# Performance work log

Measured on AMD Instinct MI355X. Metric: run time of the kernel, lower is better.

## Reference

```python
import jax, jax.numpy as jnp
import numpy as np

B, N, C, D, T = 16, 1024, 16, 64, 32  # batch, max_size, max_n_colors, inner_dim, timesteps


def setup_inputs() -> dict:
    key = jax.random.key(0)
    ks = jax.random.split(key, 16)
    s = 1.0 / np.sqrt(D)
    inp = {
        "Mvv": jax.random.randint(ks[0], (B, N, N), 0, 2).astype(jnp.float32),
        "n_colors": jax.random.randint(ks[1], (B,), 2, C + 1),
        # learned / initial states
        "v_init": jax.random.normal(ks[2], (D,)) * s,            # Normal(0,1)/sqrt(D)
        "ch0": jax.random.uniform(ks[3], (B, C, D)),             # Uniform(0,1) color init
        # recurrent GNN weights (simple tanh message-passing RNN)
        "W_v": jax.random.normal(ks[4], (D, D)) * s,
        "W_vv": jax.random.normal(ks[5], (D, D)) * s,
        "W_vc": jax.random.normal(ks[6], (D, D)) * s,
        "b_v": jnp.zeros((D,)),
        "W_c": jax.random.normal(ks[7], (D, D)) * s,
        "W_cv": jax.random.normal(ks[8], (D, D)) * s,
        "b_c": jnp.zeros((D,)),
        # vote MLP: Linear(D, D//4) -> Sigmoid -> Linear(D//4, 1)
        "W1": jax.random.normal(ks[9], (D, D // 4)) * s,
        "b1": jnp.zeros((D // 4,)),
        "W2": jax.random.normal(ks[10], (D // 4, 1)) * (1.0 / np.sqrt(D // 4)),
        "b2": jnp.zeros((1,)),
    }
    return inp


def reference(Mvv, n_colors, v_init, ch0, W_v, W_vv, W_vc, b_v, W_c, W_cv, b_c, W1, b1, W2, b2):
    # add self loops (Mvv += eye)
    A = Mvv + jnp.eye(N, dtype=Mvv.dtype)[None]
    # vectorized Mvc: Mvc[b, i, j] = 1 if j < n_colors[b]
    Mvc = jnp.broadcast_to(
        (jnp.arange(C)[None, None, :] < n_colors[:, None, None]).astype(Mvv.dtype),
        (B, N, C),
    )
    # hidden state init: v_init repeated over batch/nodes
    vh0 = jnp.broadcast_to(v_init, (B, N, D))

    def step(carry, _):
        vh, ch = carry
        v_agg = jnp.einsum("bnm,bmd->bnd", A, vh)      # neighbor aggregation
        c_agg = jnp.einsum("bnc,bcd->bnd", Mvc, ch)    # color -> vertex messages
        vh_new = jnp.tanh(vh @ W_v + v_agg @ W_vv + c_agg @ W_vc + b_v)
        cv_agg = jnp.einsum("bnc,bnd->bcd", Mvc, vh_new)  # vertex -> color messages
        ch_new = jnp.tanh(ch @ W_c + cv_agg @ W_cv + b_c)
        return (vh_new, ch_new), None

    (vh, _), _ = jax.lax.scan(step, (vh0, ch0), None, length=T)

    # vote MLP + mean over nodes + sigmoid
    vote = jax.nn.sigmoid(vh @ W1 + b1) @ W2 + b2      # [B, N, 1]
    pred = jax.nn.sigmoid(jnp.mean(vote, axis=1)).squeeze()  # [B]
    return pred
```

## Files before the change

### kernel.cpp

```cpp
#include <hip/hip_runtime.h>
#include <hip/hip_bf16.h>
#include <math.h>

#define BB 16
#define NN 1024
#define CC 16
#define DD 64
#define TT 32

typedef __bf16 bf16;
typedef __bf16 bf16x8 __attribute__((ext_vector_type(8)));
typedef __bf16 bf16x4 __attribute__((ext_vector_type(4)));
typedef float f32x4 __attribute__((ext_vector_type(4)));
typedef unsigned int u32;
typedef unsigned long long u64;
typedef u32 u32v4 __attribute__((ext_vector_type(4)));

__device__ __forceinline__ void split2(float x, bf16& h, bf16& l) {
    h = (bf16)x;
    l = (bf16)(x - (float)h);
}

__device__ __forceinline__ float fast_tanh(float x) {
    float ax = fabsf(x);
    float e = __expf(-2.f * ax);
    float t = 1.f - 2.f * e / (1.f + e);
    return copysignf(t, x);
}

__device__ __forceinline__ bf16x8 expand_bits(u32 b8) {
    u32 w[4];
    #pragma unroll
    for (int p = 0; p < 4; ++p) {
        u32 tt = b8 >> (2 * p);
        w[p] = ((tt & 1u) | ((tt & 2u) << 15)) * 0x3F80u;
    }
    u32v4 u = { w[0], w[1], w[2], w[3] };
    return __builtin_bit_cast(bf16x8, u);
}


__global__ __launch_bounds__(256) void prep_kernel(
    const float* __restrict__ Mvv, const float* __restrict__ v_init,
    const float* __restrict__ W_v, const float* __restrict__ W_vv,
    u64* __restrict__ Abits,
    bf16* __restrict__ vhHi, bf16* __restrict__ vhLo,
    bf16* __restrict__ VfHi, bf16* __restrict__ VfLo,
    bf16* __restrict__ WvTh, bf16* __restrict__ WvTl,
    bf16* __restrict__ WvvTh, bf16* __restrict__ WvvTl)
{
    int gid = blockIdx.x, tid = threadIdx.x;
    if (gid < 4096) {
        int w = tid >> 6, lane = tid & 63;
        for (int it = 0; it < 16; ++it) {
            int W = gid * 64 + w * 16 + it;
            int bb  = W >> 14;
            int row = (W >> 4) & 1023;
            int wq  = W & 15;
            float x = Mvv[(((size_t)bb << 10) + row) * 1024 + wq * 64 + lane];
            u64 m = __ballot(x != 0.0f);
            if (lane == 0) Abits[W] = m;
        }
    } else if (gid < 4608) {
        size_t idx = ((size_t)(gid - 4096) * 256 + tid) * 8;
        int d0 = (int)(idx & (DD - 1));
        bf16x8 oh, ol;
        #pragma unroll
        for (int e = 0; e < 8; ++e) { bf16 h, l; split2(v_init[d0 + e], h, l); oh[e] = h; ol[e] = l; }
        *(bf16x8*)(vhHi + idx) = oh;
        *(bf16x8*)(vhLo + idx) = ol;
    } else if (gid < 5120) {
        size_t idx = ((size_t)(gid - 4608) * 256 + tid) * 8;
        int j = (int)((idx >> 5) & 63);
        bf16 h, l; split2(v_init[j], h, l);
        bf16x8 oh, ol;
        #pragma unroll
        for (int e = 0; e < 8; ++e) { oh[e] = h; ol[e] = l; }
        *(bf16x8*)(VfHi + idx) = oh;
        *(bf16x8*)(VfLo + idx) = ol;
    } else {
        for (int e = tid; e < DD * DD; e += 256) {
            int n = e >> 6, k = e & 63;
            bf16 h, l;
            split2(W_v[k * DD + n], h, l);
            WvTh[e] = h; WvTl[e] = l;
            split2(W_vv[k * DD + n], h, l);
            WvvTh[e] = h; WvvTl[e] = l;
        }
    }
}

__global__ __launch_bounds__(512, 2) void step_kernel(
    const u64* __restrict__ Abits,
    const bf16* __restrict__ vhHi_in, const bf16* __restrict__ vhLo_in,
    const bf16* __restrict__ VfHi_in, const bf16* __restrict__ VfLo_in,
    bf16* __restrict__ vhHi_out, bf16* __restrict__ vhLo_out,
    bf16* __restrict__ VfHi_out, bf16* __restrict__ VfLo_out,
    const float* __restrict__ ch_in, float* __restrict__ ch_out,
    const float* __restrict__ part_prev, float* __restrict__ part_out,
    const int* __restrict__ n_colors,
    const float* __restrict__ Wc, const float* __restrict__ Wcv, const float* __restrict__ bc,
    const float* __restrict__ Wvc, const float* __restrict__ bv,
    const bf16* __restrict__ WvTh, const bf16* __restrict__ WvTl,
    const bf16* __restrict__ WvvTh, const bf16* __restrict__ WvvTl,
    const float* __restrict__ W1, const float* __restrict__ b1, const float* __restrict__ W2,
    float* __restrict__ partial,
    int t)
{
    __shared__ float sWc[4096];
    __shared__ float sChI[1024];
    __shared__ float sRed[512];
    __shared__ float sBc[64], sBv[64], sVs[64], sMv[64], sCs[64], sCv[64];
    __shared__ float vagg[2][64 * 65];

    int tid  = threadIdx.x;
    int b    = blockIdx.x & 15;
    int blkr = blockIdx.x >> 4;
    int m0   = blkr * 64;
    int ncol = n_colors[b];
    int d = tid & 63, q = tid >> 6;

    for (int e = tid; e < 4096; e += 512) sWc[e] = Wc[e];
    for (int e = tid; e < 1024; e += 512) sChI[e] = ch_in[(size_t)b * 1024 + e];
    if (tid < 64) { sBc[tid] = bc[tid]; sBv[tid] = bv[tid]; }

    float pr[8];
    if (t > 0) {
        #pragma unroll
        for (int j = 0; j < 8; ++j)
            pr[j] = part_prev[(size_t)b * 4096 + (q * 8 + j) * 64 + d];
    }

    int lane = tid & 63, w = tid >> 6;
    int l16 = lane & 15, lhi = lane >> 4;
    int wm = w & 1, wn = (w >> 1) & 1, wk = w >> 2;

    f32x4 acc[2][2];
    #pragma unroll
    for (int mi = 0; mi < 2; ++mi)
        #pragma unroll
        for (int nt = 0; nt < 2; ++nt) acc[mi][nt] = (f32x4){0.f, 0.f, 0.f, 0.f};

    const u64* Ab = Abits + ((size_t)b * NN + m0 + wm * 32 + l16) * 16 + wk * 8;
    const bf16* VfH = VfHi_in + (size_t)b * 65536;
    const bf16* VfL = VfLo_in + (size_t)b * 65536;

    #pragma unroll
    for (int kt = 0; kt < 4; ++kt) {
        u32v4 aw0 = *(const u32v4*)(Ab + kt * 2);
        u32v4 aw1 = *(const u32v4*)(Ab + 256 + kt * 2);
        #pragma unroll
        for (int kk = 0; kk < 4; ++kk) {
            int ks = wk * 16 + kt * 4 + kk;
            bf16x8 a0 = expand_bits((aw0[kk] >> (lhi * 8)) & 0xFFu);
            bf16x8 a1 = expand_bits((aw1[kk] >> (lhi * 8)) & 0xFFu);
            size_t fo = (size_t)ks * 2048 + (wn * 32 + l16) * 32 + lhi * 8;
            bf16x8 bh0 = *(const bf16x8*)(VfH + fo);
            bf16x8 bl0 = *(const bf16x8*)(VfL + fo);
            bf16x8 bh1 = *(const bf16x8*)(VfH + fo + 512);
            bf16x8 bl1 = *(const bf16x8*)(VfL + fo + 512);
            acc[0][0] = __builtin_amdgcn_mfma_f32_16x16x32_bf16(a0, bh0, acc[0][0], 0, 0, 0);
            acc[0][1] = __builtin_amdgcn_mfma_f32_16x16x32_bf16(a0, bh1, acc[0][1], 0, 0, 0);
            acc[1][0] = __builtin_amdgcn_mfma_f32_16x16x32_bf16(a1, bh0, acc[1][0], 0, 0, 0);
            acc[1][1] = __builtin_amdgcn_mfma_f32_16x16x32_bf16(a1, bh1, acc[1][1], 0, 0, 0);
            acc[0][0] = __builtin_amdgcn_mfma_f32_16x16x32_bf16(a0, bl0, acc[0][0], 0, 0, 0);
            acc[0][1] = __builtin_amdgcn_mfma_f32_16x16x32_bf16(a0, bl1, acc[0][1], 0, 0, 0);
            acc[1][0] = __builtin_amdgcn_mfma_f32_16x16x32_bf16(a1, bl0, acc[1][0], 0, 0, 0);
            acc[1][1] = __builtin_amdgcn_mfma_f32_16x16x32_bf16(a1, bl1, acc[1][1], 0, 0, 0);
        }
    }

    #pragma unroll
    for (int mi = 0; mi < 2; ++mi)
        #pragma unroll
        for (int nt = 0; nt < 2; ++nt)
            #pragma unroll
            for (int r = 0; r < 4; ++r)
                vagg[wk][(wm * 32 + mi * 16 + lhi * 4 + r) * 65 + wn * 32 + nt * 16 + l16] = acc[mi][nt][r];
    __syncthreads();

    if (t > 0) {
        {
            float s = 0.f;
            #pragma unroll
            for (int j = 0; j < 8; ++j) s += pr[j];
            sRed[tid] = s;
        }
        __syncthreads();
        if (tid < 64) {
            float v = 0.f;
            #pragma unroll
            for (int i = 0; i < 8; ++i) v += sRed[tid + 64 * i];
            sVs[tid] = v;
        }
        __syncthreads();
        {
            float pm = 0.f;
            #pragma unroll
            for (int j = 0; j < 8; ++j) { int k = q * 8 + j; pm += sVs[k] * Wcv[k * 64 + d]; }
            sRed[tid] = pm;
        }
        __syncthreads();
        if (tid < 64) {
            float v = 0.f;
            #pragma unroll
            for (int i = 0; i < 8; ++i) v += sRed[tid + 64 * i];
            sMv[tid] = v;
        }
        __syncthreads();
        float cn[2];
        #pragma unroll
        for (int ci = 0; ci < 2; ++ci) {
            int c = q * 2 + ci;
            float s = sBc[d] + ((c < ncol) ? sMv[d] : 0.f);
            for (int k = 0; k < 64; ++k) s += sChI[c * 64 + k] * sWc[k * 64 + d];
            cn[ci] = fast_tanh(s);
        }
        __syncthreads();
        #pragma unroll
        for (int ci = 0; ci < 2; ++ci) {
            int c = q * 2 + ci;
            sChI[c * 64 + d] = cn[ci];
            ch_out[(size_t)b * 1024 + c * 64 + d] = cn[ci];
        }
        __syncthreads();
    }
    {
        float pcs = 0.f;
        #pragma unroll
        for (int ci = 0; ci < 2; ++ci) { int c = q * 2 + ci; if (c < ncol) pcs += sChI[c * 64 + d]; }
        sRed[tid] = pcs;
    }
    __syncthreads();
    if (tid < 64) {
        float v = 0.f;
        #pragma unroll
        for (int i = 0; i < 8; ++i) v += sRed[tid + 64 * i];
        sCs[tid] = v;
    }
    __syncthreads();
    {
        float pv = 0.f;
        #pragma unroll
        for (int j = 0; j < 8; ++j) { int k = q * 8 + j; pv += sCs[k] * Wvc[k * 64 + d]; }
        sRed[tid] = pv;
    }
    __syncthreads();
    if (tid < 64) {
        float v = sBv[tid];
        #pragma unroll
        for (int i = 0; i < 8; ++i) v += sRed[tid + 64 * i];
        sCv[tid] = v;
    }
    __syncthreads();

    int rt = (w & 3) * 16, ct = (w >> 2) * 32;

    f32x4 p2[2][2];
    #pragma unroll
    for (int nt = 0; nt < 2; ++nt)
        #pragma unroll
        for (int kk = 0; kk < 2; ++kk) p2[nt][kk] = (f32x4){0.f, 0.f, 0.f, 0.f};

    #pragma unroll
    for (int kk = 0; kk < 2; ++kk) {
        int d0 = kk * 32 + lhi * 8;
        size_t vo = ((size_t)b * NN + m0 + rt + l16) * 64 + d0;
        bf16x8 a1h = *(const bf16x8*)(vhHi_in + vo);
        bf16x8 a1l = *(const bf16x8*)(vhLo_in + vo);
        int vb = (rt + l16) * 65 + d0;
        bf16x8 a2h, a2l;
        #pragma unroll
        for (int e = 0; e < 8; ++e) {
            float v = vagg[0][vb + e] + vagg[1][vb + e] + (float)a1h[e] + (float)a1l[e];
            bf16 h, l; split2(v, h, l);
            a2h[e] = h; a2l[e] = l;
        }
        #pragma unroll
        for (int nt = 0; nt < 2; ++nt) {
            int woff = (ct + nt * 16 + l16) * 64 + d0;
            bf16x8 b1h = *(const bf16x8*)(WvTh + woff);
            bf16x8 b1l = *(const bf16x8*)(WvTl + woff);
            bf16x8 b2h = *(const bf16x8*)(WvvTh + woff);
            bf16x8 b2l = *(const bf16x8*)(WvvTl + woff);
            p2[nt][kk] = __builtin_amdgcn_mfma_f32_16x16x32_bf16(a1h, b1h, p2[nt][kk], 0, 0, 0);
            p2[nt][kk] = __builtin_amdgcn_mfma_f32_16x16x32_bf16(a1l, b1h, p2[nt][kk], 0, 0, 0);
            p2[nt][kk] = __builtin_amdgcn_mfma_f32_16x16x32_bf16(a1h, b1l, p2[nt][kk], 0, 0, 0);
            p2[nt][kk] = __builtin_amdgcn_mfma_f32_16x16x32_bf16(a2h, b2h, p2[nt][kk], 0, 0, 0);
            p2[nt][kk] = __builtin_amdgcn_mfma_f32_16x16x32_bf16(a2l, b2h, p2[nt][kk], 0, 0, 0);
            p2[nt][kk] = __builtin_amdgcn_mfma_f32_16x16x32_bf16(a2h, b2l, p2[nt][kk], 0, 0, 0);
        }
    }

    float tvv[2][4];
    #pragma unroll
    for (int nt = 0; nt < 2; ++nt) {
        float cv = sCv[ct + nt * 16 + l16];
        #pragma unroll
        for (int r = 0; r < 4; ++r) tvv[nt][r] = fast_tanh(p2[nt][0][r] + p2[nt][1][r] + cv);
    }

    if (t < TT - 1) {
        int ksW = (m0 + rt) >> 5;
        int khi = 2 * ((rt >> 4) & 1) + (lhi >> 1);
        size_t vout_base = (size_t)b * NN * DD;
        #pragma unroll
        for (int nt = 0; nt < 2; ++nt) {
            int col = ct + nt * 16 + l16;
            float cs = tvv[nt][0] + tvv[nt][1] + tvv[nt][2] + tvv[nt][3];
            cs += __shfl_xor(cs, 16);
            cs += __shfl_xor(cs, 32);
            if (lhi == 0)
                part_out[(((size_t)b * 16 + blkr) * 4 + (w & 3)) * 64 + col] = cs;

            bf16x4 pkh, pkl;
            #pragma unroll
            for (int r = 0; r < 4; ++r) {
                bf16 h, l; split2(tvv[nt][r], h, l);
                pkh[r] = h; pkl[r] = l;
                size_t ro = vout_base + (size_t)(m0 + rt + lhi * 4 + r) * 64 + col;
                vhHi_out[ro] = h;
                vhLo_out[ro] = l;
            }
            size_t fo = (size_t)b * 65536 + (size_t)ksW * 2048 + col * 32 + khi * 8 + (lhi & 1) * 4;
            *(bf16x4*)(VfHi_out + fo) = pkh;
            *(bf16x4*)(VfLo_out + fo) = pkl;
        }
    } else {
        __syncthreads();
        float* sX  = &vagg[0][0];
        float* sW1 = &vagg[1][0];
        #pragma unroll
        for (int nt = 0; nt < 2; ++nt) {
            int col = ct + nt * 16 + l16;
            #pragma unroll
            for (int r = 0; r < 4; ++r)
                sX[(rt + lhi * 4 + r) * 65 + col] = tvv[nt][r];
        }
        for (int e = tid; e < 1024; e += 512) sW1[e] = W1[e];
        if (tid < 16) { sVs[tid] = W2[tid]; sMv[tid] = b1[tid]; }
        __syncthreads();

        int nl = tid & 63;
        int jq = tid >> 6;
        float h0 = sMv[jq * 2], h1 = sMv[jq * 2 + 1];
        for (int dd = 0; dd < 64; ++dd) {
            float x = sX[nl * 65 + dd];
            h0 += x * sW1[dd * 16 + jq * 2];
            h1 += x * sW1[dd * 16 + jq * 2 + 1];
        }
        float pv = sVs[jq * 2] / (1.f + __expf(-h0)) + sVs[jq * 2 + 1] / (1.f + __expf(-h1));
        sRed[tid] = pv;
        __syncthreads();
        if (tid < 64) {
            float v = 0.f;
            #pragma unroll
            for (int i = 0; i < 8; ++i) v += sRed[tid + 64 * i];
            #pragma unroll
            for (int off = 1; off < 64; off <<= 1) v += __shfl_xor(v, off);
            if (tid == 0) partial[blockIdx.x] = v;
        }
    }
}

__global__ __launch_bounds__(256) void final_reduce_kernel(
    const float* __restrict__ partial, const float* __restrict__ b2, float* __restrict__ out)
{
    int tid = threadIdx.x;
    int b = tid >> 4, p = tid & 15;
    float v = partial[p * 16 + b];
    #pragma unroll
    for (int off = 1; off < 16; off <<= 1) v += __shfl_xor(v, off);
    if (p == 0) out[b] = 1.f / (1.f + expf(-(v / 1024.f + b2[0])));
}

extern "C" void kernel_launch(void* const* d_in, const int* in_sizes, int n_in,
                              void* d_out, int out_size, void* d_ws, size_t ws_size,
                              hipStream_t stream) {
    const float* Mvv  = (const float*)d_in[0];
    const int*   ncol = (const int*)d_in[1];
    const float* vini = (const float*)d_in[2];
    const float* ch0  = (const float*)d_in[3];
    const float* W_v  = (const float*)d_in[4];
    const float* W_vv = (const float*)d_in[5];
    const float* W_vc = (const float*)d_in[6];
    const float* b_v  = (const float*)d_in[7];
    const float* W_c  = (const float*)d_in[8];
    const float* W_cv = (const float*)d_in[9];
    const float* b_c  = (const float*)d_in[10];
    const float* W1   = (const float*)d_in[11];
    const float* b1   = (const float*)d_in[12];
    const float* W2   = (const float*)d_in[13];
    const float* b2   = (const float*)d_in[14];

    char* base = (char*)d_ws;
    size_t off = 0;
    u64* Abits = (u64*)(base + off); off += (size_t)BB * NN * 16 * 8;
    const size_t SVH = (size_t)BB * NN * DD * 2;
    bf16* vhHi[2] = {(bf16*)(base + off), (bf16*)(base + off + SVH)}; off += 2 * SVH;
    bf16* vhLo[2] = {(bf16*)(base + off), (bf16*)(base + off + SVH)}; off += 2 * SVH;
    bf16* VfHi[2] = {(bf16*)(base + off), (bf16*)(base + off + SVH)}; off += 2 * SVH;
    bf16* VfLo[2] = {(bf16*)(base + off), (bf16*)(base + off + SVH)}; off += 2 * SVH;
    const size_t SCH = (size_t)BB * CC * DD * 4;
    float* chb[2] = {(float*)(base + off), (float*)(base + off + SCH)}; off += 2 * SCH;
    const size_t SPB = (size_t)BB * 64 * DD * 4;
    float* pb[2] = {(float*)(base + off), (float*)(base + off + SPB)}; off += 2 * SPB;
    bf16* WvTh  = (bf16*)(base + off); off += DD * DD * 2;
    bf16* WvTl  = (bf16*)(base + off); off += DD * DD * 2;
    bf16* WvvTh = (bf16*)(base + off); off += DD * DD * 2;
    bf16* WvvTl = (bf16*)(base + off); off += DD * DD * 2;
    float* partial = (float*)(base + off); off += 256 * 4;

    prep_kernel<<<5121, 256, 0, stream>>>(Mvv, vini, W_v, W_vv, Abits,
        vhHi[0], vhLo[0], VfHi[0], VfLo[0], WvTh, WvTl, WvvTh, WvvTl);

    for (int t = 0; t < TT; ++t) {
        const float* ch_in = (t <= 1) ? ch0 : chb[(t - 1) & 1];
        int i = t & 1, o = (t + 1) & 1;
        step_kernel<<<256, 512, 0, stream>>>(Abits,
            vhHi[i], vhLo[i], VfHi[i], VfLo[i],
            vhHi[o], vhLo[o], VfHi[o], VfLo[o],
            ch_in, chb[t & 1],
            pb[(t + 1) & 1], pb[t & 1],
            ncol, W_c, W_cv, b_c, W_vc, b_v,
            WvTh, WvTl, WvvTh, WvvTl,
            W1, b1, W2, partial, t);
    }

    final_reduce_kernel<<<1, 256, 0, stream>>>(partial, b2, (float*)d_out);
}
```

Measured before the change: 703.0 us.

## Halve rows per block and double the step kernel grid

The step kernel now handles 32 vertex rows per block instead of 64, so it launches 512 blocks instead of 256 and asks for higher occupancy in its launch bounds. The warp-to-tile mapping for the aggregation matmul and the dense-update matmul is reworked so each wave owns a single 16-column tile. The partial-sum layout and the vote reduction, including the final reduce kernel, are adjusted to match. The aim is to spread each latency-bound timestep over more waves and CUs, at the cost of repeating the per-batch colour and weight setup (Wc load, colour reductions) in twice as many blocks.

```diff
diff --git a/kernel.cpp b/kernel.cpp
--- a/kernel.cpp
+++ b/kernel.cpp
@@ -90,7 +90,7 @@
     }
 }
 
-__global__ __launch_bounds__(512, 2) void step_kernel(
+__global__ __launch_bounds__(512, 4) void step_kernel(
     const u64* __restrict__ Abits,
     const bf16* __restrict__ vhHi_in, const bf16* __restrict__ vhLo_in,
     const bf16* __restrict__ VfHi_in, const bf16* __restrict__ VfLo_in,
@@ -111,12 +111,12 @@
     __shared__ float sChI[1024];
     __shared__ float sRed[512];
     __shared__ float sBc[64], sBv[64], sVs[64], sMv[64], sCs[64], sCv[64];
-    __shared__ float vagg[2][64 * 65];
+    __shared__ float vagg[2][32 * 65];
 
     int tid  = threadIdx.x;
     int b    = blockIdx.x & 15;
     int blkr = blockIdx.x >> 4;
-    int m0   = blkr * 64;
+    int m0   = blkr * 32;
     int ncol = n_colors[b];
     int d = tid & 63, q = tid >> 6;
 
@@ -133,15 +133,13 @@
 
     int lane = tid & 63, w = tid >> 6;
     int l16 = lane & 15, lhi = lane >> 4;
-    int wm = w & 1, wn = (w >> 1) & 1, wk = w >> 2;
-
-    f32x4 acc[2][2];
-    #pragma unroll
-    for (int mi = 0; mi < 2; ++mi)
-        #pragma unroll
-        for (int nt = 0; nt < 2; ++nt) acc[mi][nt] = (f32x4){0.f, 0.f, 0.f, 0.f};
-
-    const u64* Ab = Abits + ((size_t)b * NN + m0 + wm * 32 + l16) * 16 + wk * 8;
+    int wn = w & 3, wk = w >> 2;
+
+    f32x4 acc[2];
+    acc[0] = (f32x4){0.f, 0.f, 0.f, 0.f};
+    acc[1] = (f32x4){0.f, 0.f, 0.f, 0.f};
+
+    const u64* Ab = Abits + ((size_t)b * NN + m0 + l16) * 16 + wk * 8;
     const bf16* VfH = VfHi_in + (size_t)b * 65536;
     const bf16* VfL = VfLo_in + (size_t)b * 65536;
 
@@ -154,29 +152,21 @@
             int ks = wk * 16 + kt * 4 + kk;
             bf16x8 a0 = expand_bits((aw0[kk] >> (lhi * 8)) & 0xFFu);
             bf16x8 a1 = expand_bits((aw1[kk] >> (lhi * 8)) & 0xFFu);
-            size_t fo = (size_t)ks * 2048 + (wn * 32 + l16) * 32 + lhi * 8;
-            bf16x8 bh0 = *(const bf16x8*)(VfH + fo);
-            bf16x8 bl0 = *(const bf16x8*)(VfL + fo);
-            bf16x8 bh1 = *(const bf16x8*)(VfH + fo + 512);
-            bf16x8 bl1 = *(const bf16x8*)(VfL + fo + 512);
-            acc[0][0] = __builtin_amdgcn_mfma_f32_16x16x32_bf16(a0, bh0, acc[0][0], 0, 0, 0);
-            acc[0][1] = __builtin_amdgcn_mfma_f32_16x16x32_bf16(a0, bh1, acc[0][1], 0, 0, 0);
-            acc[1][0] = __builtin_amdgcn_mfma_f32_16x16x32_bf16(a1, bh0, acc[1][0], 0, 0, 0);
-            acc[1][1] = __builtin_amdgcn_mfma_f32_16x16x32_bf16(a1, bh1, acc[1][1], 0, 0, 0);
-            acc[0][0] = __builtin_amdgcn_mfma_f32_16x16x32_bf16(a0, bl0, acc[0][0], 0, 0, 0);
-            acc[0][1] = __builtin_amdgcn_mfma_f32_16x16x32_bf16(a0, bl1, acc[0][1], 0, 0, 0);
-            acc[1][0] = __builtin_amdgcn_mfma_f32_16x16x32_bf16(a1, bl0, acc[1][0], 0, 0, 0);
-            acc[1][1] = __builtin_amdgcn_mfma_f32_16x16x32_bf16(a1, bl1, acc[1][1], 0, 0, 0);
+            size_t fo = (size_t)ks * 2048 + (wn * 16 + l16) * 32 + lhi * 8;
+            bf16x8 bh = *(const bf16x8*)(VfH + fo);
+            bf16x8 bl = *(const bf16x8*)(VfL + fo);
+            acc[0] = __builtin_amdgcn_mfma_f32_16x16x32_bf16(a0, bh, acc[0], 0, 0, 0);
+            acc[1] = __builtin_amdgcn_mfma_f32_16x16x32_bf16(a1, bh, acc[1], 0, 0, 0);
+            acc[0] = __builtin_amdgcn_mfma_f32_16x16x32_bf16(a0, bl, acc[0], 0, 0, 0);
+            acc[1] = __builtin_amdgcn_mfma_f32_16x16x32_bf16(a1, bl, acc[1], 0, 0, 0);
         }
     }
 
     #pragma unroll
     for (int mi = 0; mi < 2; ++mi)
         #pragma unroll
-        for (int nt = 0; nt < 2; ++nt)
-            #pragma unroll
-            for (int r = 0; r < 4; ++r)
-                vagg[wk][(wm * 32 + mi * 16 + lhi * 4 + r) * 65 + wn * 32 + nt * 16 + l16] = acc[mi][nt][r];
+        for (int r = 0; r < 4; ++r)
+            vagg[wk][(mi * 16 + lhi * 4 + r) * 65 + wn * 16 + l16] = acc[mi][r];
     __syncthreads();
 
     if (t > 0) {
@@ -254,13 +244,9 @@
     }
     __syncthreads();
 
-    int rt = (w & 3) * 16, ct = (w >> 2) * 32;
-
-    f32x4 p2[2][2];
-    #pragma unroll
-    for (int nt = 0; nt < 2; ++nt)
-        #pragma unroll
-        for (int kk = 0; kk < 2; ++kk) p2[nt][kk] = (f32x4){0.f, 0.f, 0.f, 0.f};
+    int rt = (w & 1) * 16, ct = (w >> 1) * 16;
+
+    f32x4 p2 = (f32x4){0.f, 0.f, 0.f, 0.f};
 
     #pragma unroll
     for (int kk = 0; kk < 2; ++kk) {
@@ -276,101 +262,84 @@
             bf16 h, l; split2(v, h, l);
             a2h[e] = h; a2l[e] = l;
         }
-        #pragma unroll
-        for (int nt = 0; nt < 2; ++nt) {
-            int woff = (ct + nt * 16 + l16) * 64 + d0;
-            bf16x8 b1h = *(const bf16x8*)(WvTh + woff);
-            bf16x8 b1l = *(const bf16x8*)(WvTl + woff);
-            bf16x8 b2h = *(const bf16x8*)(WvvTh + woff);
-            bf16x8 b2l = *(const bf16x8*)(WvvTl + woff);
-            p2[nt][kk] = __builtin_amdgcn_mfma_f32_16x16x32_bf16(a1h, b1h, p2[nt][kk], 0, 0, 0);
-            p2[nt][kk] = __builtin_amdgcn_mfma_f32_16x16x32_bf16(a1l, b1h, p2[nt][kk], 0, 0, 0);
-            p2[nt][kk] = __builtin_amdgcn_mfma_f32_16x16x32_bf16(a1h, b1l, p2[nt][kk], 0, 0, 0);
-            p2[nt][kk] = __builtin_amdgcn_mfma_f32_16x16x32_bf16(a2h, b2h, p2[nt][kk], 0, 0, 0);
-            p2[nt][kk] = __builtin_amdgcn_mfma_f32_16x16x32_bf16(a2l, b2h, p2[nt][kk], 0, 0, 0);
-            p2[nt][kk] = __builtin_amdgcn_mfma_f32_16x16x32_bf16(a2h, b2l, p2[nt][kk], 0, 0, 0);
-        }
-    }
-
-    float tvv[2][4];
-    #pragma unroll
-    for (int nt = 0; nt < 2; ++nt) {
-        float cv = sCv[ct + nt * 16 + l16];
-        #pragma unroll
-        for (int r = 0; r < 4; ++r) tvv[nt][r] = fast_tanh(p2[nt][0][r] + p2[nt][1][r] + cv);
-    }
+        int woff = (ct + l16) * 64 + d0;
+        bf16x8 b1h = *(const bf16x8*)(WvTh + woff);
+        bf16x8 b1l = *(const bf16x8*)(WvTl + woff);
+        bf16x8 b2h = *(const bf16x8*)(WvvTh + woff);
+        bf16x8 b2l = *(const bf16x8*)(WvvTl + woff);
+        p2 = __builtin_amdgcn_mfma_f32_16x16x32_bf16(a1h, b1h, p2, 0, 0, 0);
+        p2 = __builtin_amdgcn_mfma_f32_16x16x32_bf16(a1l, b1h, p2, 0, 0, 0);
+        p2 = __builtin_amdgcn_mfma_f32_16x16x32_bf16(a1h, b1l, p2, 0, 0, 0);
+        p2 = __builtin_amdgcn_mfma_f32_16x16x32_bf16(a2h, b2h, p2, 0, 0, 0);
+        p2 = __builtin_amdgcn_mfma_f32_16x16x32_bf16(a2l, b2h, p2, 0, 0, 0);
+        p2 = __builtin_amdgcn_mfma_f32_16x16x32_bf16(a2h, b2l, p2, 0, 0, 0);
+    }
+
+    int col = ct + l16;
+    float cv = sCv[col];
+    float tv[4];
+    #pragma unroll
+    for (int r = 0; r < 4; ++r) tv[r] = fast_tanh(p2[r] + cv);
 
     if (t < TT - 1) {
+        float cs = tv[0] + tv[1] + tv[2] + tv[3];
+        cs += __shfl_xor(cs, 16);
+        cs += __shfl_xor(cs, 32);
+        if (lhi == 0)
+            part_out[(size_t)b * 4096 + (blkr * 2 + (w & 1)) * 64 + col] = cs;
+
+        size_t vout_base = (size_t)b * NN * DD;
+        bf16x4 pkh, pkl;
+        #pragma unroll
+        for (int r = 0; r < 4; ++r) {
+            bf16 h, l; split2(tv[r], h, l);
+            pkh[r] = h; pkl[r] = l;
+            size_t ro = vout_base + (size_t)(m0 + rt + lhi * 4 + r) * 64 + col;
+            vhHi_out[ro] = h;
+            vhLo_out[ro] = l;
+        }
         int ksW = (m0 + rt) >> 5;
         int khi = 2 * ((rt >> 4) & 1) + (lhi >> 1);
-        size_t vout_base = (size_t)b * NN * DD;
-        #pragma unroll
-        for (int nt = 0; nt < 2; ++nt) {
-            int col = ct + nt * 16 + l16;
-            float cs = tvv[nt][0] + tvv[nt][1] + tvv[nt][2] + tvv[nt][3];
-            cs += __shfl_xor(cs, 16);
-            cs += __shfl_xor(cs, 32);
-            if (lhi == 0)
-                part_out[(((size_t)b * 16 + blkr) * 4 + (w & 3)) * 64 + col] = cs;
-
-            bf16x4 pkh, pkl;
-            #pragma unroll
-            for (int r = 0; r < 4; ++r) {
-                bf16 h, l; split2(tvv[nt][r], h, l);
-                pkh[r] = h; pkl[r] = l;
-                size_t ro = vout_base + (size_t)(m0 + rt + lhi * 4 + r) * 64 + col;
-                vhHi_out[ro] = h;
-                vhLo_out[ro] = l;
-            }
-            size_t fo = (size_t)b * 65536 + (size_t)ksW * 2048 + col * 32 + khi * 8 + (lhi & 1) * 4;
-            *(bf16x4*)(VfHi_out + fo) = pkh;
-            *(bf16x4*)(VfLo_out + fo) = pkl;
-        }
+        size_t fo = (size_t)b * 65536 + (size_t)ksW * 2048 + col * 32 + khi * 8 + (lhi & 1) * 4;
+        *(bf16x4*)(VfHi_out + fo) = pkh;
+        *(bf16x4*)(VfLo_out + fo) = pkl;
     } else {
         __syncthreads();
         float* sX  = &vagg[0][0];
         float* sW1 = &vagg[1][0];
         #pragma unroll
-        for (int nt = 0; nt < 2; ++nt) {
-            int col = ct + nt * 16 + l16;
-            #pragma unroll
-            for (int r = 0; r < 4; ++r)
-                sX[(rt + lhi * 4 + r) * 65 + col] = tvv[nt][r];
-        }
+        for (int r = 0; r < 4; ++r)
+            sX[(rt + lhi * 4 + r) * 65 + col] = tv[r];
         for (int e = tid; e < 1024; e += 512) sW1[e] = W1[e];
         if (tid < 16) { sVs[tid] = W2[tid]; sMv[tid] = b1[tid]; }
         __syncthreads();
 
-        int nl = tid & 63;
-        int jq = tid >> 6;
-        float h0 = sMv[jq * 2], h1 = sMv[jq * 2 + 1];
-        for (int dd = 0; dd < 64; ++dd) {
-            float x = sX[nl * 65 + dd];
-            h0 += x * sW1[dd * 16 + jq * 2];
-            h1 += x * sW1[dd * 16 + jq * 2 + 1];
-        }
-        float pv = sVs[jq * 2] / (1.f + __expf(-h0)) + sVs[jq * 2 + 1] / (1.f + __expf(-h1));
-        sRed[tid] = pv;
-        __syncthreads();
-        if (tid < 64) {
-            float v = 0.f;
-            #pragma unroll
-            for (int i = 0; i < 8; ++i) v += sRed[tid + 64 * i];
-            #pragma unroll
-            for (int off = 1; off < 64; off <<= 1) v += __shfl_xor(v, off);
-            if (tid == 0) partial[blockIdx.x] = v;
-        }
-    }
-}
-
-__global__ __launch_bounds__(256) void final_reduce_kernel(
+        int nl = tid & 31;
+        int jq = tid >> 5;
+        float h = sMv[jq];
+        for (int dd = 0; dd < 64; ++dd)
+            h += sX[nl * 65 + dd] * sW1[dd * 16 + jq];
+        sRed[jq * 32 + nl] = sVs[jq] / (1.f + __expf(-h));
+        __syncthreads();
+        if (tid < 32) {
+            float vote = 0.f;
+            #pragma unroll
+            for (int j = 0; j < 16; ++j) vote += sRed[j * 32 + tid];
+            #pragma unroll
+            for (int off = 1; off < 32; off <<= 1) vote += __shfl_xor(vote, off);
+            if (tid == 0) partial[blockIdx.x] = vote;
+        }
+    }
+}
+
+__global__ __launch_bounds__(512) void final_reduce_kernel(
     const float* __restrict__ partial, const float* __restrict__ b2, float* __restrict__ out)
 {
     int tid = threadIdx.x;
-    int b = tid >> 4, p = tid & 15;
+    int b = tid >> 5, p = tid & 31;
     float v = partial[p * 16 + b];
     #pragma unroll
-    for (int off = 1; off < 16; off <<= 1) v += __shfl_xor(v, off);
+    for (int off = 1; off < 32; off <<= 1) v += __shfl_xor(v, off);
     if (p == 0) out[b] = 1.f / (1.f + expf(-(v / 1024.f + b2[0])));
 }
 
@@ -409,7 +378,7 @@
     bf16* WvTl  = (bf16*)(base + off); off += DD * DD * 2;
     bf16* WvvTh = (bf16*)(base + off); off += DD * DD * 2;
     bf16* WvvTl = (bf16*)(base + off); off += DD * DD * 2;
-    float* partial = (float*)(base + off); off += 256 * 4;
+    float* partial = (float*)(base + off); off += 512 * 4;
 
     prep_kernel<<<5121, 256, 0, stream>>>(Mvv, vini, W_v, W_vv, Abits,
         vhHi[0], vhLo[0], VfHi[0], VfLo[0], WvTh, WvTl, WvvTh, WvvTl);
@@ -417,7 +386,7 @@
     for (int t = 0; t < TT; ++t) {
         const float* ch_in = (t <= 1) ? ch0 : chb[(t - 1) & 1];
         int i = t & 1, o = (t + 1) & 1;
-        step_kernel<<<256, 512, 0, stream>>>(Abits,
+        step_kernel<<<512, 512, 0, stream>>>(Abits,
             vhHi[i], vhLo[i], VfHi[i], VfLo[i],
             vhHi[o], vhLo[o], VfHi[o], VfLo[o],
             ch_in, chb[t & 1],
@@ -427,5 +396,5 @@
             W1, b1, W2, partial, t);
     }
 
-    final_reduce_kernel<<<1, 256, 0, stream>>>(partial, b2, (float*)d_out);
-}
+    final_reduce_kernel<<<1, 512, 0, stream>>>(partial, b2, (float*)d_out);
+}
```

Measured after the change: 941.6 us. +33.9%, slower.

## Compute color-state update in a single wave with shuffles instead of block-wide reductions

Applied to the files above, without the earlier changes.

Moves the per-step color hidden-state update and color-to-vertex message computation into wave 0, using register arrays and lane shuffles. This replaces the shared-memory staging of Wc, the 8-way block reductions and about ten __syncthreads barriers. It also makes only block row 0 write ch_out rather than every block. The trade-off is that one wave does all this serial work while the other waves wait at the barrier, and shared memory use drops, which may allow more blocks per CU.

```diff
diff --git a/kernel.cpp b/kernel.cpp
--- a/kernel.cpp
+++ b/kernel.cpp
@@ -107,29 +107,15 @@
     float* __restrict__ partial,
     int t)
 {
-    __shared__ float sWc[4096];
-    __shared__ float sChI[1024];
+    __shared__ float vagg[2][64 * 65];
     __shared__ float sRed[512];
-    __shared__ float sBc[64], sBv[64], sVs[64], sMv[64], sCs[64], sCv[64];
-    __shared__ float vagg[2][64 * 65];
+    __shared__ float sCv[64], sVs[64], sMv[64];
 
     int tid  = threadIdx.x;
     int b    = blockIdx.x & 15;
     int blkr = blockIdx.x >> 4;
     int m0   = blkr * 64;
     int ncol = n_colors[b];
-    int d = tid & 63, q = tid >> 6;
-
-    for (int e = tid; e < 4096; e += 512) sWc[e] = Wc[e];
-    for (int e = tid; e < 1024; e += 512) sChI[e] = ch_in[(size_t)b * 1024 + e];
-    if (tid < 64) { sBc[tid] = bc[tid]; sBv[tid] = bv[tid]; }
-
-    float pr[8];
-    if (t > 0) {
-        #pragma unroll
-        for (int j = 0; j < 8; ++j)
-            pr[j] = part_prev[(size_t)b * 4096 + (q * 8 + j) * 64 + d];
-    }
 
     int lane = tid & 63, w = tid >> 6;
     int l16 = lane & 15, lhi = lane >> 4;
@@ -177,81 +163,57 @@
             #pragma unroll
             for (int r = 0; r < 4; ++r)
                 vagg[wk][(wm * 32 + mi * 16 + lhi * 4 + r) * 65 + wn * 32 + nt * 16 + l16] = acc[mi][nt][r];
-    __syncthreads();
-
-    if (t > 0) {
-        {
-            float s = 0.f;
-            #pragma unroll
-            for (int j = 0; j < 8; ++j) s += pr[j];
-            sRed[tid] = s;
-        }
-        __syncthreads();
-        if (tid < 64) {
-            float v = 0.f;
-            #pragma unroll
-            for (int i = 0; i < 8; ++i) v += sRed[tid + 64 * i];
-            sVs[tid] = v;
-        }
-        __syncthreads();
-        {
-            float pm = 0.f;
-            #pragma unroll
-            for (int j = 0; j < 8; ++j) { int k = q * 8 + j; pm += sVs[k] * Wcv[k * 64 + d]; }
-            sRed[tid] = pm;
-        }
-        __syncthreads();
-        if (tid < 64) {
-            float v = 0.f;
-            #pragma unroll
-            for (int i = 0; i < 8; ++i) v += sRed[tid + 64 * i];
-            sMv[tid] = v;
-        }
-        __syncthreads();
-        float cn[2];
-        #pragma unroll
-        for (int ci = 0; ci < 2; ++ci) {
-            int c = q * 2 + ci;
-            float s = sBc[d] + ((c < ncol) ? sMv[d] : 0.f);
-            for (int k = 0; k < 64; ++k) s += sChI[c * 64 + k] * sWc[k * 64 + d];
-            cn[ci] = fast_tanh(s);
-        }
-        __syncthreads();
-        #pragma unroll
-        for (int ci = 0; ci < 2; ++ci) {
-            int c = q * 2 + ci;
-            sChI[c * 64 + d] = cn[ci];
-            ch_out[(size_t)b * 1024 + c * 64 + d] = cn[ci];
-        }
-        __syncthreads();
-    }
-    {
-        float pcs = 0.f;
-        #pragma unroll
-        for (int ci = 0; ci < 2; ++ci) { int c = q * 2 + ci; if (c < ncol) pcs += sChI[c * 64 + d]; }
-        sRed[tid] = pcs;
-    }
-    __syncthreads();
-    if (tid < 64) {
-        float v = 0.f;
-        #pragma unroll
-        for (int i = 0; i < 8; ++i) v += sRed[tid + 64 * i];
-        sCs[tid] = v;
-    }
-    __syncthreads();
-    {
-        float pv = 0.f;
-        #pragma unroll
-        for (int j = 0; j < 8; ++j) { int k = q * 8 + j; pv += sCs[k] * Wvc[k * 64 + d]; }
-        sRed[tid] = pv;
-    }
-    __syncthreads();
-    if (tid < 64) {
-        float v = sBv[tid];
-        #pragma unroll
-        for (int i = 0; i < 8; ++i) v += sRed[tid + 64 * i];
-        sCv[tid] = v;
-    }
+
+    if (w == 0) {
+        float chp[16];
+        #pragma unroll
+        for (int c = 0; c < 16; ++c) chp[c] = ch_in[(size_t)b * 1024 + c * 64 + lane];
+        float chn[16];
+        if (t > 0) {
+            float s0 = 0.f, s1 = 0.f, s2 = 0.f, s3 = 0.f;
+            const float* pp = part_prev + (size_t)b * 4096 + lane;
+            #pragma unroll 4
+            for (int p = 0; p < 64; p += 4) {
+                s0 += pp[(p + 0) * 64]; s1 += pp[(p + 1) * 64];
+                s2 += pp[(p + 2) * 64]; s3 += pp[(p + 3) * 64];
+            }
+            float vsum = (s0 + s1) + (s2 + s3);
+            float mv = 0.f;
+            #pragma unroll 8
+            for (int k = 0; k < 64; ++k)
+                mv += __shfl(vsum, k) * Wcv[k * 64 + lane];
+            float bcv = bc[lane];
+            float pre[16];
+            #pragma unroll
+            for (int c = 0; c < 16; ++c) pre[c] = bcv + ((c < ncol) ? mv : 0.f);
+            #pragma unroll 4
+            for (int k = 0; k < 64; ++k) {
+                float wkv = Wc[k * 64 + lane];
+                #pragma unroll
+                for (int c = 0; c < 16; ++c)
+                    pre[c] += __shfl(chp[c], k) * wkv;
+            }
+            #pragma unroll
+            for (int c = 0; c < 16; ++c) chn[c] = fast_tanh(pre[c]);
+            if (blkr == 0) {
+                #pragma unroll
+                for (int c = 0; c < 16; ++c)
+                    ch_out[(size_t)b * 1024 + c * 64 + lane] = chn[c];
+            }
+        } else {
+            #pragma unroll
+            for (int c = 0; c < 16; ++c) chn[c] = chp[c];
+        }
+        float cs = 0.f;
+        #pragma unroll
+        for (int c = 0; c < 16; ++c) if (c < ncol) cs += chn[c];
+        float cv = bv[lane];
+        #pragma unroll 8
+        for (int k = 0; k < 64; ++k)
+            cv += __shfl(cs, k) * Wvc[k * 64 + lane];
+        sCv[lane] = cv;
+    }
+
     __syncthreads();
 
     int rt = (w & 3) * 16, ct = (w >> 2) * 32;
```

Result: slower. 890.7 us (+26.7%).

## Hoist W_v MFMA early, stage vh output through LDS for coalesced stores

Applied to the files above, without the earlier changes.

Moves the vh@W_v MFMA block and its global loads ahead of the aggregation write-back and color-update phase, so that independent work overlaps with the barrier-heavy reductions. Replaces the scattered per-element bf16 stores of the new vertex state with a staging pass through shared memory, followed by 16-byte coalesced row stores. The color state is now written to global memory only by the first row block instead of by every block. The cost is two extra barriers, more live registers (a1h/a1l, p2), and reuse of the vagg shared buffer for staging.

```diff
diff --git a/kernel.cpp b/kernel.cpp
--- a/kernel.cpp
+++ b/kernel.cpp
@@ -170,6 +170,31 @@
         }
     }
 
+    int rt = (w & 3) * 16, ct = (w >> 2) * 32;
+    f32x4 p2[2][2];
+    #pragma unroll
+    for (int nt = 0; nt < 2; ++nt)
+        #pragma unroll
+        for (int kk = 0; kk < 2; ++kk) p2[nt][kk] = (f32x4){0.f, 0.f, 0.f, 0.f};
+
+    bf16x8 a1h[2], a1l[2];
+    #pragma unroll
+    for (int kk = 0; kk < 2; ++kk) {
+        int d0 = kk * 32 + lhi * 8;
+        size_t vo = ((size_t)b * NN + m0 + rt + l16) * 64 + d0;
+        a1h[kk] = *(const bf16x8*)(vhHi_in + vo);
+        a1l[kk] = *(const bf16x8*)(vhLo_in + vo);
+        #pragma unroll
+        for (int nt = 0; nt < 2; ++nt) {
+            int woff = (ct + nt * 16 + l16) * 64 + d0;
+            bf16x8 b1h = *(const bf16x8*)(WvTh + woff);
+            bf16x8 b1l = *(const bf16x8*)(WvTl + woff);
+            p2[nt][kk] = __builtin_amdgcn_mfma_f32_16x16x32_bf16(a1h[kk], b1h, p2[nt][kk], 0, 0, 0);
+            p2[nt][kk] = __builtin_amdgcn_mfma_f32_16x16x32_bf16(a1l[kk], b1h, p2[nt][kk], 0, 0, 0);
+            p2[nt][kk] = __builtin_amdgcn_mfma_f32_16x16x32_bf16(a1h[kk], b1l, p2[nt][kk], 0, 0, 0);
+        }
+    }
+
     #pragma unroll
     for (int mi = 0; mi < 2; ++mi)
         #pragma unroll
@@ -221,7 +246,8 @@
         for (int ci = 0; ci < 2; ++ci) {
             int c = q * 2 + ci;
             sChI[c * 64 + d] = cn[ci];
-            ch_out[(size_t)b * 1024 + c * 64 + d] = cn[ci];
+            if (blkr == 0)
+                ch_out[(size_t)b * 1024 + c * 64 + d] = cn[ci];
         }
         __syncthreads();
     }
@@ -254,38 +280,22 @@
     }
     __syncthreads();
 
-    int rt = (w & 3) * 16, ct = (w >> 2) * 32;
-
-    f32x4 p2[2][2];
-    #pragma unroll
-    for (int nt = 0; nt < 2; ++nt)
-        #pragma unroll
-        for (int kk = 0; kk < 2; ++kk) p2[nt][kk] = (f32x4){0.f, 0.f, 0.f, 0.f};
-
     #pragma unroll
     for (int kk = 0; kk < 2; ++kk) {
         int d0 = kk * 32 + lhi * 8;
-        size_t vo = ((size_t)b * NN + m0 + rt + l16) * 64 + d0;
-        bf16x8 a1h = *(const bf16x8*)(vhHi_in + vo);
-        bf16x8 a1l = *(const bf16x8*)(vhLo_in + vo);
         int vb = (rt + l16) * 65 + d0;
         bf16x8 a2h, a2l;
         #pragma unroll
         for (int e = 0; e < 8; ++e) {
-            float v = vagg[0][vb + e] + vagg[1][vb + e] + (float)a1h[e] + (float)a1l[e];
+            float v = vagg[0][vb + e] + vagg[1][vb + e] + (float)a1h[kk][e] + (float)a1l[kk][e];
             bf16 h, l; split2(v, h, l);
             a2h[e] = h; a2l[e] = l;
         }
         #pragma unroll
         for (int nt = 0; nt < 2; ++nt) {
             int woff = (ct + nt * 16 + l16) * 64 + d0;
-            bf16x8 b1h = *(const bf16x8*)(WvTh + woff);
-            bf16x8 b1l = *(const bf16x8*)(WvTl + woff);
             bf16x8 b2h = *(const bf16x8*)(WvvTh + woff);
             bf16x8 b2l = *(const bf16x8*)(WvvTl + woff);
-            p2[nt][kk] = __builtin_amdgcn_mfma_f32_16x16x32_bf16(a1h, b1h, p2[nt][kk], 0, 0, 0);
-            p2[nt][kk] = __builtin_amdgcn_mfma_f32_16x16x32_bf16(a1l, b1h, p2[nt][kk], 0, 0, 0);
-            p2[nt][kk] = __builtin_amdgcn_mfma_f32_16x16x32_bf16(a1h, b1l, p2[nt][kk], 0, 0, 0);
             p2[nt][kk] = __builtin_amdgcn_mfma_f32_16x16x32_bf16(a2h, b2h, p2[nt][kk], 0, 0, 0);
             p2[nt][kk] = __builtin_amdgcn_mfma_f32_16x16x32_bf16(a2l, b2h, p2[nt][kk], 0, 0, 0);
             p2[nt][kk] = __builtin_amdgcn_mfma_f32_16x16x32_bf16(a2h, b2l, p2[nt][kk], 0, 0, 0);
@@ -303,7 +313,7 @@
     if (t < TT - 1) {
         int ksW = (m0 + rt) >> 5;
         int khi = 2 * ((rt >> 4) & 1) + (lhi >> 1);
-        size_t vout_base = (size_t)b * NN * DD;
+        bf16x4 pkh[2], pkl[2];
         #pragma unroll
         for (int nt = 0; nt < 2; ++nt) {
             int col = ct + nt * 16 + l16;
@@ -313,19 +323,32 @@
             if (lhi == 0)
                 part_out[(((size_t)b * 16 + blkr) * 4 + (w & 3)) * 64 + col] = cs;
 
-            bf16x4 pkh, pkl;
             #pragma unroll
             for (int r = 0; r < 4; ++r) {
                 bf16 h, l; split2(tvv[nt][r], h, l);
-                pkh[r] = h; pkl[r] = l;
-                size_t ro = vout_base + (size_t)(m0 + rt + lhi * 4 + r) * 64 + col;
-                vhHi_out[ro] = h;
-                vhLo_out[ro] = l;
+                pkh[nt][r] = h; pkl[nt][r] = l;
             }
             size_t fo = (size_t)b * 65536 + (size_t)ksW * 2048 + col * 32 + khi * 8 + (lhi & 1) * 4;
-            *(bf16x4*)(VfHi_out + fo) = pkh;
-            *(bf16x4*)(VfLo_out + fo) = pkl;
-        }
+            *(bf16x4*)(VfHi_out + fo) = pkh[nt];
+            *(bf16x4*)(VfLo_out + fo) = pkl[nt];
+        }
+        __syncthreads();
+        bf16* sVhH = (bf16*)&vagg[0][0];
+        bf16* sVhL = sVhH + 64 * 72;
+        #pragma unroll
+        for (int nt = 0; nt < 2; ++nt) {
+            int col = ct + nt * 16 + l16;
+            #pragma unroll
+            for (int r = 0; r < 4; ++r) {
+                sVhH[(rt + lhi * 4 + r) * 72 + col] = pkh[nt][r];
+                sVhL[(rt + lhi * 4 + r) * 72 + col] = pkl[nt][r];
+            }
+        }
+        __syncthreads();
+        int row = tid >> 3, c8 = (tid & 7) * 8;
+        size_t ro = ((size_t)b * NN + m0 + row) * 64 + c8;
+        *(bf16x8*)(vhHi_out + ro) = *(bf16x8*)(sVhH + row * 72 + c8);
+        *(bf16x8*)(vhLo_out + ro) = *(bf16x8*)(sVhL + row * 72 + c8);
     } else {
         __syncthreads();
         float* sX  = &vagg[0][0];
```

Result: no change. 698.2 us, median of 3 (-0.7%).
